# Kernel tuning notes

Hardware: AMD Instinct MI355X
Metric: run time of the kernel (lower is better)

## Reference

```python
import jax, jax.numpy as jnp
import numpy as np

B, T, S, H, E, V, L = 8, 512, 1024, 64, 64, 32000, 3
SQ = float(np.sqrt(0.5))


def setup_inputs() -> dict:
    key = jax.random.key(0)
    ks = jax.random.split(key, 9)
    w = lambda k, shape: jax.random.normal(k, shape, jnp.float32) * 0.05
    return dict(
        input_x=jax.random.normal(ks[0], (B, T, E), jnp.float32),
        encoder_outputs=jax.random.normal(ks[1], (B, S, E), jnp.float32),
        encoder_attention=jax.random.normal(ks[2], (B, S, E), jnp.float32),
        W1=w(ks[3], (E, H)), b1=jnp.zeros((H,), jnp.float32),
        convW=w(ks[4], (5, H, H, 2 * H)), convb=jnp.zeros((2 * H,), jnp.float32),
        Wce=w(ks[5], (H, E)), bce=jnp.zeros((E,), jnp.float32),
        Wec=w(ks[6], (E, H)), bec=jnp.zeros((H,), jnp.float32),
        W2=w(ks[7], (H, E)), b2=jnp.zeros((E,), jnp.float32),
        W3=w(ks[8], (E, V)), b3=jnp.zeros((V,), jnp.float32),
    )


def reference(input_x, encoder_outputs, encoder_attention,
              W1, b1, convW, convb, Wce, bce, Wec, bec, W2, b2, W3, b3):
    # dropout rate is 1 - p = 0 -> identity, so dropout layers are no-ops
    attn_scale = E * np.sqrt(2.0 / E)  # encoder dim * sqrt(2/dim), per original
    dl1 = jax.nn.relu(input_x @ W1 + b1)  # [B,T,H]
    y = dl1
    # TF 'same' padding: kernel (5, H) over (batch, time) axes of [1,B,T,H]
    pad = [(2, 2), ((H - 1) // 2, H // 2)]
    for _ in range(L):
        res = y
        c = jax.lax.conv_general_dilated(
            y[None], convW, window_strides=(1, 1), padding=pad,
            dimension_numbers=('NHWC', 'HWIO', 'NHWC')) + convb  # [1,B,T,2H]
        glu = c[0, :, :, :H] * jax.nn.sigmoid(c[0, :, :, H:])     # [B,T,H]
        y = (glu + res) * SQ
        pg = jax.nn.softmax(y @ Wce + bce, axis=-1)               # [B,T,E]
        logits = jnp.einsum('bte,bse->bts', pg, encoder_attention)
        attn = jax.nn.softmax(logits, axis=2)                     # [B,T,S]
        ao = jnp.einsum('bts,bse->bte', attn, encoder_outputs) * attn_scale
        y = jax.nn.softmax(ao @ Wec + bec, axis=-1)               # [B,T,H]
    y = (y + dl1) * SQ
    out = jax.nn.relu(y @ W2 + b2)      # [B,T,E]
    out = jax.nn.relu(out @ W3 + b3)    # [B,T,V]
    return jax.nn.softmax(out, axis=2)
```

## Files before the change

kernel.cpp:

```cpp
#include <hip/hip_runtime.h>

#define NB 8
#define NT 512
#define NS 1024
#define NV 32000
#define BT 4096
#define SQH 0.70710678118654752440f
#define ATTN_SCALE 11.313708498984761f

typedef __attribute__((ext_vector_type(8))) short bf16x8;
typedef __attribute__((ext_vector_type(4))) float f32x4;
typedef unsigned short u16_t;
typedef unsigned int u32_t;

#define MFMA16(a, b, c) __builtin_amdgcn_mfma_f32_16x16x32_bf16((a), (b), (c), 0, 0, 0)

typedef __attribute__((address_space(1))) const u32_t gas_u32;
typedef __attribute__((address_space(3))) u32_t las_u32;
__device__ __forceinline__ void gld_lds16(const u16_t* g, u16_t* l){
  __builtin_amdgcn_global_load_lds((gas_u32*)g, (las_u32*)l, 16, 0, 0);
}

__device__ __forceinline__ u16_t f2bf(float f){
  union { float f; u32_t i; } v; v.f = f;
  return (u16_t)((v.i + 0x7fffu + ((v.i >> 16) & 1u)) >> 16);
}

__global__ __launch_bounds__(256) void k_prep(
    const float* __restrict__ input_x, const float* __restrict__ enc_out,
    const float* __restrict__ enc_att, const float* __restrict__ W1,
    const float* __restrict__ b1, const float* __restrict__ convW,
    const float* __restrict__ W3,
    u16_t* __restrict__ Wt, u16_t* __restrict__ W3t, float* __restrict__ dl1v,
    u16_t* __restrict__ ybf, u16_t* __restrict__ eabf, u16_t* __restrict__ eoT){
  __shared__ __align__(16) char smem[33792];
  int tid = threadIdx.x, t = blockIdx.x;

  if(t < 320){
    float (*tile)[130] = (float(*)[130])smem;
    const float* src = convW + (size_t)t * 8192;
    for(int i = tid; i < 8192; i += 256) tile[i >> 7][i & 127] = src[i];
    __syncthreads();
    u16_t* dst = Wt + (size_t)t * 8192;
    for(int i = tid; i < 8192; i += 256){
      int oc = i >> 6;
      int ic = (((i & 63) << 1) ^ ((oc & 7) << 4)) >> 1;
      dst[i] = f2bf(tile[ic][oc]);
    }
  } else if(t < 448){
    int blk = t - 320;
    int b = blk >> 4, s0 = (blk & 15) << 6;
    float (*tile)[65] = (float(*)[65])smem;
    const float* easrc = enc_att + ((size_t)b * NS + s0) * 64;
    u16_t* eadst = eabf + ((size_t)b * NS + s0) * 64;
    for(int i = tid; i < 512; i += 256){
      float4 f0 = *(const float4*)(easrc + i * 8);
      float4 f1 = *(const float4*)(easrc + i * 8 + 4);
      union { u32_t u[4]; bf16x8 v; } pk;
      pk.u[0] = f2bf(f0.x) | ((u32_t)f2bf(f0.y) << 16);
      pk.u[1] = f2bf(f0.z) | ((u32_t)f2bf(f0.w) << 16);
      pk.u[2] = f2bf(f1.x) | ((u32_t)f2bf(f1.y) << 16);
      pk.u[3] = f2bf(f1.z) | ((u32_t)f2bf(f1.w) << 16);
      *(bf16x8*)(eadst + i * 8) = pk.v;
    }
    const float* eosrc = enc_out + ((size_t)b * NS + s0) * 64;
    for(int i = tid; i < 1024; i += 256){
      int s = i >> 4, e0 = (i & 15) * 4;
      float4 f = *(const float4*)(eosrc + s * 64 + e0);
      tile[s][e0] = f.x; tile[s][e0 + 1] = f.y; tile[s][e0 + 2] = f.z; tile[s][e0 + 3] = f.w;
    }
    __syncthreads();
    for(int i = tid; i < 512; i += 256){
      int e = i >> 3, sc = (i & 7) * 8;
      union { u32_t u[4]; bf16x8 v; } pk;
      #pragma unroll
      for(int j = 0; j < 4; j++){
        float lo = tile[sc + 2 * j][e], hi = tile[sc + 2 * j + 1][e];
        pk.u[j] = f2bf(lo) | ((u32_t)f2bf(hi) << 16);
      }
      *(bf16x8*)(eoT + ((size_t)b * 64 + e) * NS + s0 + sc) = pk.v;
    }
  } else if(t < 573){
    u32_t (*lt)[33] = (u32_t(*)[33])smem;
    int v0 = (t - 448) * 256;
    for(int it = 0; it < 8; it++){
      int u = it * 256 + tid;
      int rp = u >> 6;
      int c4 = (u & 63) * 4;
      const float* r0p = W3 + (size_t)(2 * rp) * NV + v0 + c4;
      float4 a4 = *(const float4*)r0p;
      float4 b4 = *(const float4*)(r0p + NV);
      lt[c4 + 0][rp] = f2bf(a4.x) | ((u32_t)f2bf(b4.x) << 16);
      lt[c4 + 1][rp] = f2bf(a4.y) | ((u32_t)f2bf(b4.y) << 16);
      lt[c4 + 2][rp] = f2bf(a4.z) | ((u32_t)f2bf(b4.z) << 16);
      lt[c4 + 3][rp] = f2bf(a4.w) | ((u32_t)f2bf(b4.w) << 16);
    }
    __syncthreads();
    u32_t* dst = (u32_t*)(W3t + (size_t)v0 * 64);
    for(int it = 0; it < 32; it++){
      int idx = it * 256 + tid;
      dst[idx] = lt[idx >> 5][idx & 31];
    }
  } else if(t < 701){
    int i = (t - 573) * 256 + tid;
    int b = i >> 12, rem = i & 4095;
    int pr = rem >> 6, c = rem & 63;
    int row = pr < 31 ? pr : pr + 512;
    ybf[((size_t)b * 576 + row) * 64 + c] = 0;
  } else {
    int r0 = (t - 701) * 4;
    float (*xs)[64] = (float(*)[64])smem;
    xs[tid >> 6][tid & 63] = input_x[(size_t)r0 * 64 + tid];
    __syncthreads();
    int h = tid & 63, rr = tid >> 6;
    float acc = b1[h];
    #pragma unroll 16
    for(int e = 0; e < 64; e++) acc = fmaf(xs[rr][e], W1[e * 64 + h], acc);
    float v = fmaxf(acc, 0.f);
    int row = r0 + rr;
    dl1v[(size_t)row * 64 + h] = v;
    ybf[((size_t)(row >> 9) * 576 + (row & 511) + 31) * 64 + h] = f2bf(v);
  }
}

__global__ __launch_bounds__(256) void k_conv(const u16_t* __restrict__ ybf,
                                              const u16_t* __restrict__ Wt,
                                              float* __restrict__ part){
  int mt = blockIdx.x;
  int khh = blockIdx.y;
  int kh = khh >> 1, half = khh & 1;
  int b = mt >> 3, t0 = (mt & 7) << 6;
  int bp = b + kh - 2;
  if(bp < 0 || bp >= NB) return;
  __shared__ u16_t strip[95 * 72];
  __shared__ u16_t wtile[2][8192];
  int tid = threadIdx.x;
  int lane = tid & 63, wid = tid >> 6;
  int l15 = lane & 15, lgp = lane >> 4;

  const u16_t* ysrc = ybf + ((size_t)bp * 576 + t0 + half * 32) * 64;
  for(int li = tid; li < 760; li += 256)
    *(bf16x8*)(strip + (li >> 3) * 72 + (li & 7) * 8) = *(const bf16x8*)(ysrc + li * 8);

  const u16_t* wsrc = Wt + ((size_t)kh * 64 + half * 32) * 8192;
  {
    const u16_t* g = wsrc + tid * 8;
    #pragma unroll
    for(int j = 0; j < 4; j++)
      gld_lds16(g + j * 2048, &wtile[0][j * 2048 + wid * 512]);
  }
  __syncthreads();

  int wm = wid >> 1, wn = wid & 1;
  f32x4 acc[2][4];
  #pragma unroll
  for(int m = 0; m < 2; m++)
    #pragma unroll
    for(int n = 0; n < 4; n++) acc[m][n] = (f32x4){0.f, 0.f, 0.f, 0.f};
  int arow0 = wm * 32 + l15;

  int qoff[2][4];
  #pragma unroll
  for(int ks = 0; ks < 2; ks++)
    #pragma unroll
    for(int nf = 0; nf < 4; nf++){
      int oc = wn * 64 + nf * 16 + l15;
      int byte = (oc << 7) | (((ks << 6) | (lgp << 4)) ^ ((oc & 7) << 4));
      qoff[ks][nf] = byte >> 1;
    }

  for(int kw = 0; kw < 32; kw++){
    int cur = kw & 1;
    if(kw < 31){
      const u16_t* g = wsrc + (size_t)(kw + 1) * 8192 + tid * 8;
      #pragma unroll
      for(int j = 0; j < 4; j++)
        gld_lds16(g + j * 2048, &wtile[cur ^ 1][j * 2048 + wid * 512]);
      asm volatile("s_waitcnt vmcnt(4)" ::: "memory");
    } else {
      asm volatile("s_waitcnt vmcnt(0)" ::: "memory");
    }
    __builtin_amdgcn_s_barrier();
    const u16_t* wt = wtile[cur];
    #pragma unroll
    for(int ks = 0; ks < 2; ks++){
      bf16x8 a0 = *(const bf16x8*)(strip + (arow0 + kw) * 72 + ks * 32 + lgp * 8);
      bf16x8 a1 = *(const bf16x8*)(strip + (arow0 + 16 + kw) * 72 + ks * 32 + lgp * 8);
      bf16x8 q0 = *(const bf16x8*)(wt + qoff[ks][0]);
      bf16x8 q1 = *(const bf16x8*)(wt + qoff[ks][1]);
      bf16x8 q2 = *(const bf16x8*)(wt + qoff[ks][2]);
      bf16x8 q3 = *(const bf16x8*)(wt + qoff[ks][3]);
      acc[0][0] = MFMA16(a0, q0, acc[0][0]);
      acc[0][1] = MFMA16(a0, q1, acc[0][1]);
      acc[0][2] = MFMA16(a0, q2, acc[0][2]);
      acc[0][3] = MFMA16(a0, q3, acc[0][3]);
      acc[1][0] = MFMA16(a1, q0, acc[1][0]);
      acc[1][1] = MFMA16(a1, q1, acc[1][1]);
      acc[1][2] = MFMA16(a1, q2, acc[1][2]);
      acc[1][3] = MFMA16(a1, q3, acc[1][3]);
    }
    asm volatile("s_waitcnt lgkmcnt(0)" ::: "memory");
    __builtin_amdgcn_s_barrier();
  }

  float* dst = part + ((size_t)khh * BT + (size_t)mt * 64) * 128;
  #pragma unroll
  for(int mf = 0; mf < 2; mf++)
    #pragma unroll
    for(int nf = 0; nf < 4; nf++)
      #pragma unroll
      for(int r = 0; r < 4; r++){
        int row = wm * 32 + mf * 16 + lgp * 4 + r;
        int col = wn * 64 + nf * 16 + l15;
        dst[row * 128 + col] = acc[mf][nf][r];
      }
}

__global__ __launch_bounds__(256) void k_attn(const float* __restrict__ part,
    const float* __restrict__ convb, const float* __restrict__ ycur,
    const u16_t* __restrict__ eabf, const u16_t* __restrict__ eoT,
    const float* __restrict__ Wce, const float* __restrict__ bce,
    const float* __restrict__ Wec, const float* __restrict__ bec,
    float* __restrict__ ynext, u16_t* __restrict__ ybf){
  int row0 = blockIdx.x << 3;
  int b = row0 >> 9;
  int tid = threadIdx.x;
  int lane = tid & 63, w = tid >> 6;
  int l15 = lane & 15, lgp = lane >> 4;

  __shared__ float yml[8][68];
  __shared__ float pgS[8][68];
  __shared__ u16_t pgb[16][72];
  __shared__ float aof[4][64][17];
  __shared__ float aosm[8][68];
  __shared__ float reds[4][16];
  __shared__ float invt[8];

  for(int i = tid; i < 512; i += 256) pgb[8 + (i >> 6)][i & 63] = 0;

  for(int i = tid; i < 512; i += 256){
    int r = i >> 6, h = i & 63;
    int grow = row0 + r;
    float ca = convb[h], cb = convb[64 + h];
    #pragma unroll
    for(int pp = 0; pp < 10; pp++){
      int bpp = b + (pp >> 1) - 2;
      if(bpp >= 0 && bpp < NB){
        const float* p = part + ((size_t)pp * BT + grow) * 128;
        ca += p[h]; cb += p[64 + h];
      }
    }
    float sig = 1.f / (1.f + __expf(-cb));
    yml[r][h] = (ca * sig + ycur[(size_t)grow * 64 + h]) * SQH;
  }
  __syncthreads();
  {
    int h = tid & 63, g = tid >> 6;
    float a0 = bce[h], a1 = a0;
    #pragma unroll 16
    for(int e = 0; e < 64; e++){
      float wv = Wce[e * 64 + h];
      a0 = fmaf(yml[g * 2 + 0][e], wv, a0);
      a1 = fmaf(yml[g * 2 + 1][e], wv, a1);
    }
    pgS[g * 2 + 0][h] = a0; pgS[g * 2 + 1][h] = a1;
  }
  __syncthreads();
  {
    int r = tid >> 5, j = tid & 31;
    float v1 = __expf(pgS[r][j]), v2 = __expf(pgS[r][j + 32]);
    float s = v1 + v2;
    s += __shfl_xor(s, 1); s += __shfl_xor(s, 2); s += __shfl_xor(s, 4);
    s += __shfl_xor(s, 8); s += __shfl_xor(s, 16);
    float inv = 1.f / s;
    pgb[r][j] = f2bf(v1 * inv); pgb[r][j + 32] = f2bf(v2 * inv);
  }
  __syncthreads();

  bf16x8 qpg0 = *(const bf16x8*)&pgb[l15][lgp * 8];
  bf16x8 qpg1 = *(const bf16x8*)&pgb[l15][32 + lgp * 8];
  float sumacc = 0.f;
  f32x4 ao[4];
  #pragma unroll
  for(int et = 0; et < 4; et++) ao[et] = (f32x4){0.f, 0.f, 0.f, 0.f};
  const u16_t* eab = eabf + ((size_t)b * NS + w * 256) * 64;
  const u16_t* eob = eoT + (size_t)b * 64 * NS + w * 256;
  for(int sc = 0; sc < 8; sc++){
    int sb = sc * 32;
    const u16_t* ar = eab + (size_t)(sb + l15) * 64 + lgp * 8;
    bf16x8 a00 = *(const bf16x8*)ar;
    bf16x8 a01 = *(const bf16x8*)(ar + 32);
    bf16x8 a10 = *(const bf16x8*)(ar + 1024);
    bf16x8 a11 = *(const bf16x8*)(ar + 1024 + 32);
    f32x4 s0 = {0.f, 0.f, 0.f, 0.f}, s1 = {0.f, 0.f, 0.f, 0.f};
    s0 = MFMA16(a00, qpg0, s0); s0 = MFMA16(a01, qpg1, s0);
    s1 = MFMA16(a10, qpg0, s1); s1 = MFMA16(a11, qpg1, s1);
    float p00 = __expf(s0[0]), p01 = __expf(s0[1]), p02 = __expf(s0[2]), p03 = __expf(s0[3]);
    float p10 = __expf(s1[0]), p11 = __expf(s1[1]), p12 = __expf(s1[2]), p13 = __expf(s1[3]);
    sumacc += (p00 + p01) + (p02 + p03) + (p10 + p11) + (p12 + p13);
    u32_t A0, B0, A1, B1;
    asm("v_cvt_pk_bf16_f32 %0, %1, %2" : "=v"(A0) : "v"(p00), "v"(p01));
    asm("v_cvt_pk_bf16_f32 %0, %1, %2" : "=v"(B0) : "v"(p02), "v"(p03));
    asm("v_cvt_pk_bf16_f32 %0, %1, %2" : "=v"(A1) : "v"(p10), "v"(p11));
    asm("v_cvt_pk_bf16_f32 %0, %1, %2" : "=v"(B1) : "v"(p12), "v"(p13));
    int src0 = l15 + ((lgp & 1) << 5);
    int src1 = src0 + 16;
    u32_t w0a = (u32_t)__shfl((int)A0, src0, 64), w0b = (u32_t)__shfl((int)A1, src0, 64);
    u32_t w1a = (u32_t)__shfl((int)B0, src0, 64), w1b = (u32_t)__shfl((int)B1, src0, 64);
    u32_t w2a = (u32_t)__shfl((int)A0, src1, 64), w2b = (u32_t)__shfl((int)A1, src1, 64);
    u32_t w3a = (u32_t)__shfl((int)B0, src1, 64), w3b = (u32_t)__shfl((int)B1, src1, 64);
    bool hi = lgp >= 2;
    union { u32_t u[4]; bf16x8 v; } bav;
    bav.u[0] = hi ? w0b : w0a; bav.u[1] = hi ? w1b : w1a;
    bav.u[2] = hi ? w2b : w2a; bav.u[3] = hi ? w3b : w3a;
    #pragma unroll
    for(int et = 0; et < 4; et++){
      const u16_t* er = eob + (size_t)(et * 16 + l15) * NS + sb + lgp * 8;
      bf16x8 ae = *(const bf16x8*)er;
      ao[et] = MFMA16(ae, bav.v, ao[et]);
    }
  }
  sumacc += __shfl_xor(sumacc, 16);
  sumacc += __shfl_xor(sumacc, 32);
  if(lane < 16) reds[w][l15] = sumacc;
  #pragma unroll
  for(int et = 0; et < 4; et++)
    #pragma unroll
    for(int r = 0; r < 4; r++)
      aof[w][et * 16 + lgp * 4 + r][l15] = ao[et][r];
  __syncthreads();
  if(tid < 8) invt[tid] = ATTN_SCALE / (reds[0][tid] + reds[1][tid] + reds[2][tid] + reds[3][tid]);
  __syncthreads();
  for(int i = tid; i < 512; i += 256){
    int e = i >> 3, t = i & 7;
    aosm[t][e] = (aof[0][e][t] + aof[1][e][t] + aof[2][e][t] + aof[3][e][t]) * invt[t];
  }
  __syncthreads();
  {
    int h = tid & 63, g = tid >> 6;
    float a0 = bec[h], a1 = a0;
    #pragma unroll 16
    for(int e = 0; e < 64; e++){
      float wv = Wec[e * 64 + h];
      a0 = fmaf(aosm[g * 2 + 0][e], wv, a0);
      a1 = fmaf(aosm[g * 2 + 1][e], wv, a1);
    }
    pgS[g * 2 + 0][h] = a0; pgS[g * 2 + 1][h] = a1;
  }
  __syncthreads();
  {
    int r = tid >> 5, j = tid & 31;
    float v1 = __expf(pgS[r][j]), v2 = __expf(pgS[r][j + 32]);
    float s = v1 + v2;
    s += __shfl_xor(s, 1); s += __shfl_xor(s, 2); s += __shfl_xor(s, 4);
    s += __shfl_xor(s, 8); s += __shfl_xor(s, 16);
    float inv = 1.f / s;
    float o1 = v1 * inv, o2 = v2 * inv;
    int grow = row0 + r;
    ynext[(size_t)grow * 64 + j] = o1;
    ynext[(size_t)grow * 64 + j + 32] = o2;
    size_t yb = ((size_t)(grow >> 9) * 576 + (grow & 511) + 31) * 64;
    ybf[yb + j] = f2bf(o1);
    ybf[yb + j + 32] = f2bf(o2);
  }
}

__global__ void k_w2(const float* __restrict__ y3, const float* __restrict__ dl1v,
                     const float* __restrict__ W2, const float* __restrict__ b2,
                     u16_t* __restrict__ y2bf, float* __restrict__ esum){
  int r0 = blockIdx.x * 4, tid = threadIdx.x;
  __shared__ float xs[4][64];
  xs[tid >> 6][tid & 63] = (y3[(size_t)r0 * 64 + tid] + dl1v[(size_t)r0 * 64 + tid]) * SQH;
  __syncthreads();
  int h = tid & 63, rr = tid >> 6;
  float acc = b2[h];
  #pragma unroll 16
  for(int e = 0; e < 64; e++) acc = fmaf(xs[rr][e], W2[e * 64 + h], acc);
  y2bf[(size_t)(r0 + rr) * 64 + h] = f2bf(fmaxf(acc, 0.f));
  if(tid < 4) esum[r0 + tid] = 0.f;
}

__global__ __launch_bounds__(256) void k_va(const u16_t* __restrict__ y2bf,
    const u16_t* __restrict__ W3t, const float* __restrict__ b3, float* __restrict__ esum){
  int m0 = blockIdx.x << 6, ns = blockIdx.y;
  int tid = threadIdx.x, lane = tid & 63, w = tid >> 6;
  int l15 = lane & 15, lgp = lane >> 4;
  bf16x8 a[4][2];
  #pragma unroll
  for(int mg = 0; mg < 4; mg++){
    const u16_t* ar = y2bf + ((size_t)(m0 + mg * 16 + l15) << 6) + lgp * 8;
    a[mg][0] = *(const bf16x8*)ar;
    a[mg][1] = *(const bf16x8*)(ar + 32);
  }
  float sums[4][4];
  #pragma unroll
  for(int mg = 0; mg < 4; mg++)
    #pragma unroll
    for(int r = 0; r < 4; r++) sums[mg][r] = 0.f;

  int nb0 = ns * 1600 + w * 400;
  for(int fi = 0; fi < 25; fi++){
    int n = nb0 + fi * 16 + l15;
    const u16_t* bp2 = W3t + ((size_t)n << 6) + lgp * 8;
    bf16x8 q0 = *(const bf16x8*)bp2;
    bf16x8 q1 = *(const bf16x8*)(bp2 + 32);
    float bias = b3[n];
    #pragma unroll
    for(int mg = 0; mg < 4; mg++){
      f32x4 acc = {0.f, 0.f, 0.f, 0.f};
      acc = MFMA16(a[mg][0], q0, acc);
      acc = MFMA16(a[mg][1], q1, acc);
      #pragma unroll
      for(int r = 0; r < 4; r++){
        float z = fmaxf(acc[r] + bias, 0.f);
        sums[mg][r] += __expf(z);
      }
    }
  }
  #pragma unroll
  for(int mg = 0; mg < 4; mg++)
    #pragma unroll
    for(int r = 0; r < 4; r++){
      float v = sums[mg][r];
      v += __shfl_xor(v, 1); v += __shfl_xor(v, 2);
      v += __shfl_xor(v, 4); v += __shfl_xor(v, 8);
      if(l15 == 0) atomicAdd(&esum[m0 + mg * 16 + lgp * 4 + r], v);
    }
}

__global__ __launch_bounds__(256) void k_vb(const u16_t* __restrict__ y2bf,
    const u16_t* __restrict__ W3t, const float* __restrict__ b3,
    const float* __restrict__ esum, float* __restrict__ out){
  int m0 = blockIdx.x << 6, ns = blockIdx.y;
  int tid = threadIdx.x, lane = tid & 63, w = tid >> 6;
  int l15 = lane & 15, lgp = lane >> 4;
  __shared__ float obuf[64][84];
  bf16x8 a[4][2];
  #pragma unroll
  for(int mg = 0; mg < 4; mg++){
    const u16_t* ar = y2bf + ((size_t)(m0 + mg * 16 + l15) << 6) + lgp * 8;
    a[mg][0] = *(const bf16x8*)ar;
    a[mg][1] = *(const bf16x8*)(ar + 32);
  }
  float invs[4][4];
  #pragma unroll
  for(int mg = 0; mg < 4; mg++)
    #pragma unroll
    for(int r = 0; r < 4; r++) invs[mg][r] = 1.f / esum[m0 + mg * 16 + lgp * 4 + r];

  int cb0 = ns * 1600;
  for(int si = 0; si < 25; si++){
    int cb = cb0 + si * 64;
    int n = cb + w * 16 + l15;
    const u16_t* bp2 = W3t + ((size_t)n << 6) + lgp * 8;
    bf16x8 q0 = *(const bf16x8*)bp2;
    bf16x8 q1 = *(const bf16x8*)(bp2 + 32);
    float bias = b3[n];
    #pragma unroll
    for(int mg = 0; mg < 4; mg++){
      f32x4 acc = {0.f, 0.f, 0.f, 0.f};
      acc = MFMA16(a[mg][0], q0, acc);
      acc = MFMA16(a[mg][1], q1, acc);
      #pragma unroll
      for(int r = 0; r < 4; r++){
        float z = fmaxf(acc[r] + bias, 0.f);
        obuf[mg * 16 + lgp * 4 + r][w * 16 + l15] = __expf(z) * invs[mg][r];
      }
    }
    __syncthreads();
    #pragma unroll
    for(int p = 0; p < 4; p++){
      int row = p * 16 + (tid >> 4);
      float4 v = *(const float4*)&obuf[row][(tid & 15) * 4];
      *(float4*)&out[(size_t)(m0 + row) * NV + cb + (tid & 15) * 4] = v;
    }
    __syncthreads();
  }
}

extern "C" void kernel_launch(void* const* d_in, const int* in_sizes, int n_in,
                              void* d_out, int out_size, void* d_ws, size_t ws_size,
                              hipStream_t stream){
  const float* input_x = (const float*)d_in[0];
  const float* enc_out = (const float*)d_in[1];
  const float* enc_att = (const float*)d_in[2];
  const float* W1    = (const float*)d_in[3];
  const float* b1    = (const float*)d_in[4];
  const float* convW = (const float*)d_in[5];
  const float* convb = (const float*)d_in[6];
  const float* Wce   = (const float*)d_in[7];
  const float* bce   = (const float*)d_in[8];
  const float* Wec   = (const float*)d_in[9];
  const float* bec   = (const float*)d_in[10];
  const float* W2    = (const float*)d_in[11];
  const float* b2    = (const float*)d_in[12];
  const float* W3    = (const float*)d_in[13];
  const float* b3    = (const float*)d_in[14];

  char* ws = (char*)d_ws;
  u16_t* Wt    = (u16_t*)(ws);
  u16_t* W3t   = (u16_t*)(ws + 5242880);
  float* dl1v  = (float*)(ws + 9338880);
  float* yB    = (float*)(ws + 11436032);
  u16_t* ybf   = (u16_t*)(ws + 12484608);
  float* part  = (float*)(ws + 13074432);
  u16_t* y2bf  = (u16_t*)(ws + 34045952);
  float* esum  = (float*)(ws + 34570240);
  u16_t* eabf  = (u16_t*)(ws + 34586624);
  u16_t* eoT   = (u16_t*)(ws + 35635200);
  float* outp  = (float*)d_out;

  k_prep<<<dim3(1725), dim3(256), 0, stream>>>(input_x, enc_out, enc_att, W1, b1,
                                               convW, W3, Wt, W3t, dl1v, ybf, eabf, eoT);

  const float* ycur = dl1v;
  for(int it = 0; it < 3; it++){
    k_conv<<<dim3(64, 10), dim3(256), 0, stream>>>(ybf, Wt, part);
    k_attn<<<dim3(512), dim3(256), 0, stream>>>(part, convb, ycur, eabf, eoT,
                                                Wce, bce, Wec, bec, yB, ybf);
    ycur = yB;
  }

  k_w2<<<dim3(1024), dim3(256), 0, stream>>>(yB, dl1v, W2, b2, y2bf, esum);
  k_va<<<dim3(64, 20), dim3(256), 0, stream>>>(y2bf, W3t, b3, esum);
  k_vb<<<dim3(64, 20), dim3(256), 0, stream>>>(y2bf, W3t, b3, esum, outp);
}
```

Baseline: 314.7 us.

## Split conv reduction into quarter chunks and fuse W2 projection into last attention pass

The conv kernel now splits the kw reduction into four 16-step chunks per kernel row instead of two 32-step halves, doubling the grid to raise occupancy and shorten each block's serial loop. The attention kernel sums 20 partial buffers instead of 10. On the final layer it also computes the residual add, the W2 projection and the ReLU in place, which removes the separate k_w2 launch and its round trip through global memory. The cost is twice the partial-sum buffer size and twice the traffic in the attention reduction, and the workspace offsets are shifted to make room.

```diff
diff --git a/kernel.cpp b/kernel.cpp
--- a/kernel.cpp
+++ b/kernel.cpp
@@ -128,21 +128,21 @@
                                               float* __restrict__ part){
   int mt = blockIdx.x;
   int khh = blockIdx.y;
-  int kh = khh >> 1, half = khh & 1;
+  int kh = khh >> 2, q = khh & 3;
   int b = mt >> 3, t0 = (mt & 7) << 6;
   int bp = b + kh - 2;
   if(bp < 0 || bp >= NB) return;
-  __shared__ u16_t strip[95 * 72];
+  __shared__ u16_t strip[79 * 72];
   __shared__ u16_t wtile[2][8192];
   int tid = threadIdx.x;
   int lane = tid & 63, wid = tid >> 6;
   int l15 = lane & 15, lgp = lane >> 4;
 
-  const u16_t* ysrc = ybf + ((size_t)bp * 576 + t0 + half * 32) * 64;
-  for(int li = tid; li < 760; li += 256)
+  const u16_t* ysrc = ybf + ((size_t)bp * 576 + t0 + q * 16) * 64;
+  for(int li = tid; li < 632; li += 256)
     *(bf16x8*)(strip + (li >> 3) * 72 + (li & 7) * 8) = *(const bf16x8*)(ysrc + li * 8);
 
-  const u16_t* wsrc = Wt + ((size_t)kh * 64 + half * 32) * 8192;
+  const u16_t* wsrc = Wt + ((size_t)kh * 64 + q * 16) * 8192;
   {
     const u16_t* g = wsrc + tid * 8;
     #pragma unroll
@@ -169,9 +169,9 @@
       qoff[ks][nf] = byte >> 1;
     }
 
-  for(int kw = 0; kw < 32; kw++){
+  for(int kw = 0; kw < 16; kw++){
     int cur = kw & 1;
-    if(kw < 31){
+    if(kw < 15){
       const u16_t* g = wsrc + (size_t)(kw + 1) * 8192 + tid * 8;
       #pragma unroll
       for(int j = 0; j < 4; j++)
@@ -221,7 +221,10 @@
     const u16_t* __restrict__ eabf, const u16_t* __restrict__ eoT,
     const float* __restrict__ Wce, const float* __restrict__ bce,
     const float* __restrict__ Wec, const float* __restrict__ bec,
-    float* __restrict__ ynext, u16_t* __restrict__ ybf){
+    float* __restrict__ ynext, u16_t* __restrict__ ybf,
+    const float* __restrict__ dl1v, const float* __restrict__ W2,
+    const float* __restrict__ b2, u16_t* __restrict__ y2bf,
+    float* __restrict__ esum, int L){
   int row0 = blockIdx.x << 3;
   int b = row0 >> 9;
   int tid = threadIdx.x;
@@ -243,8 +246,8 @@
     int grow = row0 + r;
     float ca = convb[h], cb = convb[64 + h];
     #pragma unroll
-    for(int pp = 0; pp < 10; pp++){
-      int bpp = b + (pp >> 1) - 2;
+    for(int pp = 0; pp < 20; pp++){
+      int bpp = b + (pp >> 2) - 2;
       if(bpp >= 0 && bpp < NB){
         const float* p = part + ((size_t)pp * BT + grow) * 128;
         ca += p[h]; cb += p[64 + h];
@@ -356,28 +359,37 @@
     s += __shfl_xor(s, 8); s += __shfl_xor(s, 16);
     float inv = 1.f / s;
     float o1 = v1 * inv, o2 = v2 * inv;
-    int grow = row0 + r;
-    ynext[(size_t)grow * 64 + j] = o1;
-    ynext[(size_t)grow * 64 + j + 32] = o2;
-    size_t yb = ((size_t)(grow >> 9) * 576 + (grow & 511) + 31) * 64;
-    ybf[yb + j] = f2bf(o1);
-    ybf[yb + j + 32] = f2bf(o2);
-  }
-}
-
-__global__ void k_w2(const float* __restrict__ y3, const float* __restrict__ dl1v,
-                     const float* __restrict__ W2, const float* __restrict__ b2,
-                     u16_t* __restrict__ y2bf, float* __restrict__ esum){
-  int r0 = blockIdx.x * 4, tid = threadIdx.x;
-  __shared__ float xs[4][64];
-  xs[tid >> 6][tid & 63] = (y3[(size_t)r0 * 64 + tid] + dl1v[(size_t)r0 * 64 + tid]) * SQH;
-  __syncthreads();
-  int h = tid & 63, rr = tid >> 6;
-  float acc = b2[h];
-  #pragma unroll 16
-  for(int e = 0; e < 64; e++) acc = fmaf(xs[rr][e], W2[e * 64 + h], acc);
-  y2bf[(size_t)(r0 + rr) * 64 + h] = f2bf(fmaxf(acc, 0.f));
-  if(tid < 4) esum[r0 + tid] = 0.f;
+    if(L < 2){
+      int grow = row0 + r;
+      ynext[(size_t)grow * 64 + j] = o1;
+      ynext[(size_t)grow * 64 + j + 32] = o2;
+      size_t yb = ((size_t)(grow >> 9) * 576 + (grow & 511) + 31) * 64;
+      ybf[yb + j] = f2bf(o1);
+      ybf[yb + j + 32] = f2bf(o2);
+    } else {
+      yml[r][j] = o1;
+      yml[r][j + 32] = o2;
+    }
+  }
+  if(L == 2){
+    __syncthreads();
+    for(int i = tid; i < 512; i += 256){
+      int r = i >> 6, h = i & 63;
+      pgS[r][h] = (yml[r][h] + dl1v[(size_t)(row0 + r) * 64 + h]) * SQH;
+    }
+    __syncthreads();
+    int h = tid & 63, g = tid >> 6;
+    float a0 = b2[h], a1 = a0;
+    #pragma unroll 16
+    for(int e = 0; e < 64; e++){
+      float wv = W2[e * 64 + h];
+      a0 = fmaf(pgS[g * 2 + 0][e], wv, a0);
+      a1 = fmaf(pgS[g * 2 + 1][e], wv, a1);
+    }
+    y2bf[(size_t)(row0 + g * 2 + 0) * 64 + h] = f2bf(fmaxf(a0, 0.f));
+    y2bf[(size_t)(row0 + g * 2 + 1) * 64 + h] = f2bf(fmaxf(a1, 0.f));
+    if(tid < 8) esum[row0 + tid] = 0.f;
+  }
 }
 
 __global__ __launch_bounds__(256) void k_va(const u16_t* __restrict__ y2bf,
@@ -501,13 +513,13 @@
   u16_t* Wt    = (u16_t*)(ws);
   u16_t* W3t   = (u16_t*)(ws + 5242880);
   float* dl1v  = (float*)(ws + 9338880);
-  float* yB    = (float*)(ws + 11436032);
-  u16_t* ybf   = (u16_t*)(ws + 12484608);
-  float* part  = (float*)(ws + 13074432);
-  u16_t* y2bf  = (u16_t*)(ws + 34045952);
-  float* esum  = (float*)(ws + 34570240);
-  u16_t* eabf  = (u16_t*)(ws + 34586624);
-  u16_t* eoT   = (u16_t*)(ws + 35635200);
+  float* yB    = (float*)(ws + 10387456);
+  u16_t* ybf   = (u16_t*)(ws + 11436032);
+  float* part  = (float*)(ws + 12025856);
+  u16_t* y2bf  = (u16_t*)(ws + 53968896);
+  float* esum  = (float*)(ws + 54493184);
+  u16_t* eabf  = (u16_t*)(ws + 54509568);
+  u16_t* eoT   = (u16_t*)(ws + 55558144);
   float* outp  = (float*)d_out;
 
   k_prep<<<dim3(1725), dim3(256), 0, stream>>>(input_x, enc_out, enc_att, W1, b1,
@@ -515,13 +527,13 @@
 
   const float* ycur = dl1v;
   for(int it = 0; it < 3; it++){
-    k_conv<<<dim3(64, 10), dim3(256), 0, stream>>>(ybf, Wt, part);
+    k_conv<<<dim3(64, 20), dim3(256), 0, stream>>>(ybf, Wt, part);
     k_attn<<<dim3(512), dim3(256), 0, stream>>>(part, convb, ycur, eabf, eoT,
-                                                Wce, bce, Wec, bec, yB, ybf);
+                                                Wce, bce, Wec, bec, yB, ybf,
+                                                dl1v, W2, b2, y2bf, esum, it);
     ycur = yB;
   }
 
-  k_w2<<<dim3(1024), dim3(256), 0, stream>>>(yB, dl1v, W2, b2, y2bf, esum);
   k_va<<<dim3(64, 20), dim3(256), 0, stream>>>(y2bf, W3t, b3, esum);
   k_vb<<<dim3(64, 20), dim3(256), 0, stream>>>(y2bf, W3t, b3, esum, outp);
 }
```

After: 334.4 us. +6.3%, slower.
